# Performance work log

Hardware: AMD Instinct MI355X
Metric: run time of the kernel (lower is better)

Reference implementation:

```python
import jax, jax.numpy as jnp
import numpy as np

N_NODES = 50000
N_FEAT = 128
N_HIDDEN = 256
N_CLASSES = 1
N_EDGES = 800000


def gcn_layer(x, src, dst, W, b, n_nodes):
    """GCNConv: D^-1/2 (A + I) D^-1/2 X W + b, via gather-scatter over edges."""
    h = x @ W  # [N, out]
    # add self loops
    loop = jnp.arange(n_nodes, dtype=src.dtype)
    s = jnp.concatenate([src, loop])
    d = jnp.concatenate([dst, loop])
    deg = jax.ops.segment_sum(jnp.ones_like(d, dtype=h.dtype), d, num_segments=n_nodes)
    inv_sqrt = jax.lax.rsqrt(jnp.maximum(deg, 1.0))
    norm = inv_sqrt[s] * inv_sqrt[d]  # [E+N]
    msgs = h[s] * norm[:, None]       # gather: [E+N, out]
    out = jax.ops.segment_sum(msgs, d, num_segments=n_nodes)  # scatter-add
    return out + b


def setup_inputs() -> dict:
    key = jax.random.key(0)
    k1, k2, k3, k4 = jax.random.split(key, 4)
    x = jax.random.normal(k1, (N_NODES, N_FEAT), dtype=jnp.float32)
    edge_index = jax.random.randint(k2, (2, N_EDGES), 0, N_NODES, dtype=jnp.int32)
    s1 = 1.0 / np.sqrt(N_FEAT)
    s2 = 1.0 / np.sqrt(N_HIDDEN)
    W1 = jax.random.uniform(k3, (N_FEAT, N_HIDDEN), jnp.float32, -s1, s1)
    b1 = jnp.zeros((N_HIDDEN,), jnp.float32)
    W2 = jax.random.uniform(k4, (N_HIDDEN, N_CLASSES), jnp.float32, -s2, s2)
    b2 = jnp.zeros((N_CLASSES,), jnp.float32)
    return {"x": x, "edge_index": edge_index, "W1": W1, "b1": b1, "W2": W2, "b2": b2}


def reference(x, edge_index, W1, b1, W2, b2):
    src, dst = edge_index[0], edge_index[1]
    n = x.shape[0]
    h = gcn_layer(x, src, dst, W1, b1, n)
    h = jax.nn.relu(h)  # dropout=0.0 -> identity
    out = gcn_layer(h, src, dst, W2, b2, n)
    return out  # [N, n_classes]
```

## Files before the change

kernel.cpp:

```cpp
#include <hip/hip_runtime.h>

typedef unsigned int uint;
typedef unsigned short ushort;
typedef __attribute__((ext_vector_type(8))) short short8;
typedef __attribute__((ext_vector_type(4))) float f32x4;

#define CAP   64
#define BM16  16
#define STR   68
#define NPB   192
#define NBIN  261
#define CAPB  4096
#define EPB   4096

__device__ __forceinline__ float bf_lo(uint p) { return __uint_as_float(p << 16); }
__device__ __forceinline__ float bf_hi(uint p) { return __uint_as_float(p & 0xffff0000u); }
__device__ __forceinline__ uint rne_lo(uint u) { return (u + 0x7fffu + ((u >> 16) & 1u)) >> 16; }
__device__ __forceinline__ uint rne_hi(uint u) { return (u + 0x7fffu + ((u >> 16) & 1u)) & 0xffff0000u; }

__global__ __launch_bounds__(1024) void k_part(
    const int* __restrict__ src, const int* __restrict__ dst,
    int* __restrict__ binCnt, uint* __restrict__ binData, int E,
    const float* __restrict__ W1, uint* __restrict__ wpack) {
  __shared__ int hist[NBIN];
  __shared__ int base[NBIN];
  int t = threadIdx.x;

  int gid = blockIdx.x * 1024 + t;
  if (gid < 4096) {
    int kk = gid >> 10, rem = gid & 1023, ntile = rem >> 6, ln = rem & 63;
    int quad = ln >> 4, nn = ntile * 16 + (ln & 15);
    uint d[4];
#pragma unroll
    for (int jp = 0; jp < 4; ++jp) {
      int k = kk * 32 + quad * 8 + 2 * jp;
      uint lov = rne_lo(__float_as_uint(W1[k * 256 + nn]));
      uint hiv = rne_hi(__float_as_uint(W1[(k + 1) * 256 + nn]));
      d[jp] = lov | hiv;
    }
    *(uint4*)&wpack[gid * 4] = make_uint4(d[0], d[1], d[2], d[3]);
  }

  for (int i = t; i < NBIN; i += 1024) hist[i] = 0;
  __syncthreads();
  int s[4], d[4], b[4];
  bool v[4];
#pragma unroll
  for (int j = 0; j < 4; ++j) {
    int e = blockIdx.x * EPB + j * 1024 + t;
    v[j] = e < E;
    if (v[j]) {
      s[j] = src[e];
      d[j] = dst[e];
      b[j] = d[j] / NPB;
      atomicAdd(&hist[b[j]], 1);
    }
  }
  __syncthreads();
  for (int i = t; i < NBIN; i += 1024) {
    int h = hist[i];
    base[i] = h ? atomicAdd(&binCnt[i], h) : 0;
    hist[i] = 0;
  }
  __syncthreads();
#pragma unroll
  for (int j = 0; j < 4; ++j) {
    if (v[j]) {
      int r = atomicAdd(&hist[b[j]], 1);
      int idx = base[b[j]] + r;
      if (idx < CAPB)
        binData[b[j] * CAPB + idx] = (uint)s[j] | ((uint)d[j] << 16);
    }
  }
}

__global__ __launch_bounds__(1024) void k_bucketize(
    const uint* __restrict__ binData, const int* __restrict__ binCnt,
    ushort* __restrict__ col, int* __restrict__ cnt, int N,
    const float2* __restrict__ x2, uint* __restrict__ xs, float* __restrict__ inv) {
  __shared__ ushort col_l[NPB * CAP];
  __shared__ int cnt_l[NPB];
  int b = blockIdx.x, t = threadIdx.x;
  int lo = b * NPB;
  for (int i = t; i < NPB; i += 1024) cnt_l[i] = 0;
  uint* clz = (uint*)col_l;
  for (int i = t; i < NPB * (CAP / 2); i += 1024) clz[i] = 0;
  __syncthreads();
  int m = min(binCnt[b], CAPB);
  const uint* bd = &binData[b * CAPB];
  for (int e = t; e < m; e += 1024) {
    uint pr = bd[e];
    int sv = pr & 0xffffu;
    int dl = (int)(pr >> 16) - lo;
    int p = atomicAdd(&cnt_l[dl], 1);
    if (p < CAP) col_l[dl * CAP + p] = (ushort)sv;
  }
  __syncthreads();
  int nh = min(NPB, N - lo);
  if (nh <= 0) return;
  for (int i = t; i < nh; i += 1024) {
    int c = cnt_l[i];
    cnt[lo + i] = c;
    inv[lo + i] = rsqrtf((float)(c + 1));
  }
  uint* cg = (uint*)(col + (size_t)lo * CAP);
  const uint* cl = (const uint*)col_l;
  int nu = nh * (CAP / 2);
  for (int i = t; i < nu; i += 1024) cg[i] = cl[i];
  int nc = nh << 6;
  const float2* xb = x2 + ((size_t)lo << 6);
  uint* xo = xs + ((size_t)lo << 6);
  for (int i = t; i < nc; i += 1024) {
    float iv = rsqrtf((float)(cnt_l[i >> 6] + 1));
    float2 f = xb[i];
    xo[i] = rne_lo(__float_as_uint(iv * f.x)) | rne_hi(__float_as_uint(iv * f.y));
  }
}

__global__ __launch_bounds__(256, 3) void k_agg_gemm(
    const uint* __restrict__ xs, const ushort* __restrict__ col,
    const int* __restrict__ cnt, const float* __restrict__ inv,
    const uint* __restrict__ wpack, const float* __restrict__ b1,
    const float* __restrict__ W2, float* __restrict__ cz, int N) {
  __shared__ uint As[BM16 * STR];
  __shared__ float red[64];
  int t = threadIdx.x, wave = t >> 6, lane = t & 63;
  int m0 = blockIdx.x * BM16;

  int e4[4], ce4[4];
  float2 ac[4];
  float invd[4];
#pragma unroll
  for (int r = 0; r < 4; ++r) {
    int node = m0 + wave * 4 + r;
    if (node < N) {
      uint pd = xs[(size_t)node * 64 + lane];
      ac[r].x = bf_lo(pd);
      ac[r].y = bf_hi(pd);
      e4[r] = min(cnt[node], CAP);
      ce4[r] = (int)col[(size_t)node * CAP + lane];
      invd[r] = inv[node];
    } else {
      e4[r] = 0; ce4[r] = 0; invd[r] = 0.f;
      ac[r] = make_float2(0.f, 0.f);
    }
  }
  int emax = max(max(e4[0], e4[1]), max(e4[2], e4[3]));
  for (int p = 0; p < emax; p += 8) {
    uint pv[4][8];
#pragma unroll
    for (int r = 0; r < 4; ++r) {
      if (p < e4[r]) {
#pragma unroll
        for (int j = 0; j < 8; ++j) {
          int s = __shfl(ce4[r], p + j);
          pv[r][j] = xs[(size_t)s * 64 + lane];
        }
      }
    }
#pragma unroll
    for (int r = 0; r < 4; ++r) {
      if (p < e4[r]) {
        int lim = e4[r] - p;
#pragma unroll
        for (int j = 0; j < 8; ++j) {
          uint v = (j < lim) ? pv[r][j] : 0u;
          ac[r].x += bf_lo(v);
          ac[r].y += bf_hi(v);
        }
      }
    }
  }
#pragma unroll
  for (int r = 0; r < 4; ++r) {
    float axx = ac[r].x * invd[r];
    float ayy = ac[r].y * invd[r];
    As[(wave * 4 + r) * STR + lane] =
        rne_lo(__float_as_uint(axx)) | rne_hi(__float_as_uint(ayy));
  }
  __syncthreads();

  int quad = lane >> 4, mrow = lane & 15;
  f32x4 acc[4];
#pragma unroll
  for (int nt = 0; nt < 4; ++nt) acc[nt] = (f32x4){0.f, 0.f, 0.f, 0.f};
#pragma unroll
  for (int kk = 0; kk < 4; ++kk) {
    short8 af = *(const short8*)&As[mrow * STR + kk * 16 + quad * 4];
#pragma unroll
    for (int nt = 0; nt < 4; ++nt) {
      int ntile = wave * 4 + nt;
      short8 bf = *(const short8*)&wpack[((kk * 16 + ntile) * 64 + lane) * 4];
      acc[nt] = __builtin_amdgcn_mfma_f32_16x16x32_bf16(af, bf, acc[nt], 0, 0, 0);
    }
  }

  float partial[4] = {0.f, 0.f, 0.f, 0.f};
#pragma unroll
  for (int nt = 0; nt < 4; ++nt) {
    int c = (wave * 4 + nt) * 16 + mrow;
    float b1c = b1[c], w2c = W2[c];
#pragma unroll
    for (int r = 0; r < 4; ++r) {
      float h = fmaxf(acc[nt][r] + b1c, 0.f);
      partial[r] = fmaf(h, w2c, partial[r]);
    }
  }
#pragma unroll
  for (int r = 0; r < 4; ++r) {
    float p = partial[r];
    p += __shfl_xor(p, 1); p += __shfl_xor(p, 2);
    p += __shfl_xor(p, 4); p += __shfl_xor(p, 8);
    if (mrow == 0) red[wave * 16 + quad * 4 + r] = p;
  }
  __syncthreads();
  if (t < 16) {
    int node = m0 + t;
    if (node < N) {
      float s = red[t] + red[16 + t] + red[32 + t] + red[48 + t];
      cz[node] = inv[node] * s;
    }
  }
}

__global__ void k_agg2(const ushort* __restrict__ col, const int* __restrict__ cnt,
                       const float* __restrict__ cz, const float* __restrict__ b2,
                       float* __restrict__ out, int N) {
  int g = blockIdx.x * blockDim.x + threadIdx.x;
  int node = g >> 2, q = g & 3;
  if (node >= N) return;
  int e = min(cnt[node], CAP);
  float acc = (q == 0) ? cz[node] : 0.f;
  const ushort* cp = &col[node * CAP];
  for (int p = q; p < e; p += 4) acc += cz[cp[p]];
  acc += __shfl_xor(acc, 1);
  acc += __shfl_xor(acc, 2);
  if (q == 0) out[node] = rsqrtf((float)(cnt[node] + 1)) * acc + b2[0];
}

extern "C" void kernel_launch(void* const* d_in, const int* in_sizes, int n_in,
                              void* d_out, int out_size, void* d_ws, size_t ws_size,
                              hipStream_t stream) {
  const float2* x2 = (const float2*)d_in[0];
  const int*    ei = (const int*)d_in[1];
  const float*  W1 = (const float*)d_in[2];
  const float*  b1 = (const float*)d_in[3];
  const float*  W2 = (const float*)d_in[4];
  const float*  b2 = (const float*)d_in[5];
  int N = in_sizes[0] / 128;
  int E = in_sizes[1] / 2;
  const int* src = ei;
  const int* dst = ei + E;
  float* out = (float*)d_out;

  char* w = (char*)d_ws;
  size_t o = 0;
  auto carve = [&](size_t bytes) { char* p = w + o; o += (bytes + 255) & ~(size_t)255; return p; };
  int*    binCnt  = (int*)   carve((size_t)NBIN * 4);
  int*    cnt     = (int*)   carve((size_t)N * 4);
  uint*   binData = (uint*)  carve((size_t)NBIN * CAPB * 4);
  ushort* col     = (ushort*)carve((size_t)N * CAP * 2);
  uint*   xs      = (uint*)  carve((size_t)N * 64 * 4);
  float*  inv     = (float*) carve((size_t)N * 4);
  uint*   wpack   = (uint*)  carve(16384 * 4);
  float*  cz      = (float*) carve((size_t)N * 4);

  hipMemsetAsync(binCnt, 0, (size_t)NBIN * sizeof(int), stream);

  int nblk_p = (E + EPB - 1) / EPB;
  k_part<<<nblk_p, 1024, 0, stream>>>(src, dst, binCnt, binData, E, W1, wpack);

  k_bucketize<<<NBIN, 1024, 0, stream>>>(binData, binCnt, col, cnt, N, x2, xs, inv);

  k_agg_gemm<<<(N + BM16 - 1) / BM16, 256, 0, stream>>>(
      xs, col, cnt, inv, wpack, b1, W2, cz, N);

  long long tot2 = (long long)N * 4;
  k_agg2<<<(int)((tot2 + 255) / 256), 256, 0, stream>>>(col, cnt, cz, b2, out, N);
}
```

Baseline: 147.2 us.

## Switch bf16 storage to fp16 with packed half accumulation and f16 MFMA

Replaces bf16 packing and manual rounding with fp16 conversion for X, W1 and the aggregation buffer. The neighbor sum now accumulates in packed half2 adds instead of two fp32 adds, and the GEMM uses the f16 MFMA. It also uses readlane instead of shfl for neighbor indices, keeps the rank from the first histogram atomic so the second atomic pass goes away, and raises the occupancy hint to 4. Accumulating up to 64 neighbors in fp16 loses precision and risks overflow or accuracy error compared with fp32 accumulation.

```diff
diff --git a/kernel.cpp b/kernel.cpp
--- a/kernel.cpp
+++ b/kernel.cpp
@@ -2,7 +2,8 @@
 
 typedef unsigned int uint;
 typedef unsigned short ushort;
-typedef __attribute__((ext_vector_type(8))) short short8;
+typedef __attribute__((ext_vector_type(2))) _Float16 h2;
+typedef __attribute__((ext_vector_type(8))) _Float16 h8;
 typedef __attribute__((ext_vector_type(4))) float f32x4;
 
 #define CAP   64
@@ -13,10 +14,10 @@
 #define CAPB  4096
 #define EPB   4096
 
-__device__ __forceinline__ float bf_lo(uint p) { return __uint_as_float(p << 16); }
-__device__ __forceinline__ float bf_hi(uint p) { return __uint_as_float(p & 0xffff0000u); }
-__device__ __forceinline__ uint rne_lo(uint u) { return (u + 0x7fffu + ((u >> 16) & 1u)) >> 16; }
-__device__ __forceinline__ uint rne_hi(uint u) { return (u + 0x7fffu + ((u >> 16) & 1u)) & 0xffff0000u; }
+__device__ __forceinline__ uint pack_h2(float a, float b) {
+  h2 v = {(_Float16)a, (_Float16)b};
+  return __builtin_bit_cast(uint, v);
+}
 
 __global__ __launch_bounds__(1024) void k_part(
     const int* __restrict__ src, const int* __restrict__ dst,
@@ -30,20 +31,18 @@
   if (gid < 4096) {
     int kk = gid >> 10, rem = gid & 1023, ntile = rem >> 6, ln = rem & 63;
     int quad = ln >> 4, nn = ntile * 16 + (ln & 15);
-    uint d[4];
+    uint w[4];
 #pragma unroll
     for (int jp = 0; jp < 4; ++jp) {
       int k = kk * 32 + quad * 8 + 2 * jp;
-      uint lov = rne_lo(__float_as_uint(W1[k * 256 + nn]));
-      uint hiv = rne_hi(__float_as_uint(W1[(k + 1) * 256 + nn]));
-      d[jp] = lov | hiv;
-    }
-    *(uint4*)&wpack[gid * 4] = make_uint4(d[0], d[1], d[2], d[3]);
+      w[jp] = pack_h2(W1[k * 256 + nn], W1[(k + 1) * 256 + nn]);
+    }
+    *(uint4*)&wpack[gid * 4] = make_uint4(w[0], w[1], w[2], w[3]);
   }
 
   for (int i = t; i < NBIN; i += 1024) hist[i] = 0;
   __syncthreads();
-  int s[4], d[4], b[4];
+  int s[4], d[4], b[4], r[4];
   bool v[4];
 #pragma unroll
   for (int j = 0; j < 4; ++j) {
@@ -53,21 +52,19 @@
       s[j] = src[e];
       d[j] = dst[e];
       b[j] = d[j] / NPB;
-      atomicAdd(&hist[b[j]], 1);
+      r[j] = atomicAdd(&hist[b[j]], 1);
     }
   }
   __syncthreads();
   for (int i = t; i < NBIN; i += 1024) {
     int h = hist[i];
     base[i] = h ? atomicAdd(&binCnt[i], h) : 0;
-    hist[i] = 0;
   }
   __syncthreads();
 #pragma unroll
   for (int j = 0; j < 4; ++j) {
     if (v[j]) {
-      int r = atomicAdd(&hist[b[j]], 1);
-      int idx = base[b[j]] + r;
+      int idx = base[b[j]] + r[j];
       if (idx < CAPB)
         binData[b[j] * CAPB + idx] = (uint)s[j] | ((uint)d[j] << 16);
     }
@@ -113,11 +110,11 @@
   for (int i = t; i < nc; i += 1024) {
     float iv = rsqrtf((float)(cnt_l[i >> 6] + 1));
     float2 f = xb[i];
-    xo[i] = rne_lo(__float_as_uint(iv * f.x)) | rne_hi(__float_as_uint(iv * f.y));
-  }
-}
-
-__global__ __launch_bounds__(256, 3) void k_agg_gemm(
+    xo[i] = pack_h2(iv * f.x, iv * f.y);
+  }
+}
+
+__global__ __launch_bounds__(256, 4) void k_agg_gemm(
     const uint* __restrict__ xs, const ushort* __restrict__ col,
     const int* __restrict__ cnt, const float* __restrict__ inv,
     const uint* __restrict__ wpack, const float* __restrict__ b1,
@@ -128,21 +125,20 @@
   int m0 = blockIdx.x * BM16;
 
   int e4[4], ce4[4];
-  float2 ac[4];
+  h2 ac[4];
   float invd[4];
 #pragma unroll
   for (int r = 0; r < 4; ++r) {
     int node = m0 + wave * 4 + r;
     if (node < N) {
       uint pd = xs[(size_t)node * 64 + lane];
-      ac[r].x = bf_lo(pd);
-      ac[r].y = bf_hi(pd);
+      ac[r] = __builtin_bit_cast(h2, pd);
       e4[r] = min(cnt[node], CAP);
       ce4[r] = (int)col[(size_t)node * CAP + lane];
       invd[r] = inv[node];
     } else {
       e4[r] = 0; ce4[r] = 0; invd[r] = 0.f;
-      ac[r] = make_float2(0.f, 0.f);
+      ac[r] = (h2){(_Float16)0.f, (_Float16)0.f};
     }
   }
   int emax = max(max(e4[0], e4[1]), max(e4[2], e4[3]));
@@ -153,7 +149,7 @@
       if (p < e4[r]) {
 #pragma unroll
         for (int j = 0; j < 8; ++j) {
-          int s = __shfl(ce4[r], p + j);
+          int s = __builtin_amdgcn_readlane(ce4[r], p + j);
           pv[r][j] = xs[(size_t)s * 64 + lane];
         }
       }
@@ -164,19 +160,17 @@
         int lim = e4[r] - p;
 #pragma unroll
         for (int j = 0; j < 8; ++j) {
-          uint v = (j < lim) ? pv[r][j] : 0u;
-          ac[r].x += bf_lo(v);
-          ac[r].y += bf_hi(v);
+          uint u = (j < lim) ? pv[r][j] : 0u;
+          ac[r] += __builtin_bit_cast(h2, u);
         }
       }
     }
   }
 #pragma unroll
   for (int r = 0; r < 4; ++r) {
-    float axx = ac[r].x * invd[r];
-    float ayy = ac[r].y * invd[r];
-    As[(wave * 4 + r) * STR + lane] =
-        rne_lo(__float_as_uint(axx)) | rne_hi(__float_as_uint(ayy));
+    _Float16 iv = (_Float16)invd[r];
+    h2 aa = ac[r] * (h2){iv, iv};
+    As[(wave * 4 + r) * STR + lane] = __builtin_bit_cast(uint, aa);
   }
   __syncthreads();
 
@@ -186,12 +180,12 @@
   for (int nt = 0; nt < 4; ++nt) acc[nt] = (f32x4){0.f, 0.f, 0.f, 0.f};
 #pragma unroll
   for (int kk = 0; kk < 4; ++kk) {
-    short8 af = *(const short8*)&As[mrow * STR + kk * 16 + quad * 4];
+    h8 af = *(const h8*)&As[mrow * STR + kk * 16 + quad * 4];
 #pragma unroll
     for (int nt = 0; nt < 4; ++nt) {
       int ntile = wave * 4 + nt;
-      short8 bf = *(const short8*)&wpack[((kk * 16 + ntile) * 64 + lane) * 4];
-      acc[nt] = __builtin_amdgcn_mfma_f32_16x16x32_bf16(af, bf, acc[nt], 0, 0, 0);
+      h8 bf = *(const h8*)&wpack[((kk * 16 + ntile) * 64 + lane) * 4];
+      acc[nt] = __builtin_amdgcn_mfma_f32_16x16x32_f16(af, bf, acc[nt], 0, 0, 0);
     }
   }
 
```

Measured after the change: 141.9 us. -3.6%, faster.
